# Optimization experiments

Measured on AMD Instinct MI355X. Metric: run time of the kernel, lower is better.

Reference implementation:

```python
import jax, jax.numpy as jnp
import numpy as np

B, T, C = 4, 2048, 1024
H, D = 16, 64  # num_heads, head_size; H*D == C


def setup_inputs() -> dict:
    key = jax.random.key(0)
    kx, kq, kk, kv = jax.random.split(key, 4)
    x = jax.random.normal(kx, (B, T, C), dtype=jnp.float32)
    # Per-head bias-free Q/K/V projection weights, stacked over heads.
    # Scale like torch Linear default init (~1/sqrt(fan_in)).
    s = 1.0 / np.sqrt(C)
    Wq = jax.random.normal(kq, (H, C, D), dtype=jnp.float32) * s
    Wk = jax.random.normal(kk, (H, C, D), dtype=jnp.float32) * s
    Wv = jax.random.normal(kv, (H, C, D), dtype=jnp.float32) * s
    return {"x": x, "Wq": Wq, "Wk": Wk, "Wv": Wv}


def reference(x, Wq, Wk, Wv):
    # Batched equivalent of the per-head Python loop:
    # each head: q = x @ Wq[h]; k = x @ Wk[h]; v = x @ Wv[h]
    q = jnp.einsum("btc,hcd->bhtd", x, Wq)
    k = jnp.einsum("bsc,hcd->bhsd", x, Wk)
    v = jnp.einsum("bsc,hcd->bhsd", x, Wv)
    scale = 1.0 / jnp.sqrt(jnp.asarray(D, dtype=x.dtype))
    scores = jnp.einsum("bhtd,bhsd->bhts", q, k) * scale  # [B,H,T,T]
    causal = jnp.tril(jnp.ones((T, T), dtype=bool))
    scores = jnp.where(causal[None, None], scores, jnp.asarray(-jnp.inf, scores.dtype))
    attn = jax.nn.softmax(scores, axis=-1)  # dropout=0 (inference)
    out = jnp.einsum("bhts,bhsd->bhtd", attn, v)
    # Concatenate heads on the last dim (head 0 first), matching torch.cat.
    return out.transpose(0, 2, 1, 3).reshape(B, T, H * D)
```

## Files before the change

### kernel.cpp

```cpp
#include <hip/hip_runtime.h>
#include <hip/hip_bf16.h>


typedef __attribute__((ext_vector_type(8))) short short8;
typedef __attribute__((ext_vector_type(4))) float f32x4;
typedef __attribute__((ext_vector_type(16))) float f32x16;

#define XB_OFF  64
#define WT_OFF  (64 + 8388608)
#define QKV_OFF (64 + 8388608 + 3145728)

__device__ __forceinline__ short f2bf(float f) {
    union { float f; unsigned u; } un; un.f = f;
    unsigned r = un.u + 0x7fffu + ((un.u >> 16) & 1u);
    return (short)(r >> 16);
}
__device__ __forceinline__ float bf2f(short v) {
    union { unsigned u; float f; } un; un.u = ((unsigned)(unsigned short)v) << 16;
    return un.f;
}
__device__ __forceinline__ unsigned cvtpk_bf16(float lo, float hi) {
    unsigned r;
    asm("v_cvt_pk_bf16_f32 %0, %1, %2" : "=v"(r) : "v"(lo), "v"(hi));
    return r;
}
__device__ __forceinline__ float fast_exp2(float x) {
    return __builtin_amdgcn_exp2f(x);
}

__device__ __forceinline__ int swz(int row, int colByte) {
    return row * 144 + (colByte ^ ((row & 56) << 1));
}

#define GLOAD16(gsrc, ldst)                                                       \
    __builtin_amdgcn_global_load_lds(                                             \
        (const __attribute__((address_space(1))) void*)(gsrc),                    \
        (__attribute__((address_space(3))) void*)(ldst), 16, 0, 0)

__global__ __launch_bounds__(256) void detect_dtype(const unsigned short* __restrict__ xs,
                                                    int* __restrict__ flag) {
    __shared__ int red[256];
    int t = threadIdx.x, cnt = 0;
    for (int i = t; i < 8192; i += 256) {
        unsigned e = (xs[i] >> 7) & 0xFFu;
        if (e >= 0xC0u) cnt++;
    }
    red[t] = cnt;
    __syncthreads();
    for (int s = 128; s > 0; s >>= 1) { if (t < s) red[t] += red[t + s]; __syncthreads(); }
    if (t == 0) flag[0] = (red[0] > 16) ? 1 : 0;
}

__global__ __launch_bounds__(256) void convert_x(const void* __restrict__ xin,
                                                 const int* __restrict__ flag,
                                                 short* __restrict__ xb) {
    const bool isf = (flag[0] != 0);
    const int n8 = 8388608 / 8;
    int i = blockIdx.x * 256 + threadIdx.x;
    const int stride = gridDim.x * 256;
    for (; i < n8; i += stride) {
        short8 v;
        if (isf) {
            const f32x4* xf = (const f32x4*)xin + i * 2;
            f32x4 a = xf[0], b = xf[1];
#pragma unroll
            for (int j = 0; j < 4; ++j) { v[j] = f2bf(a[j]); v[4 + j] = f2bf(b[j]); }
        } else {
            v = ((const short8*)xin)[i];
        }
        ((short8*)xb)[i] = v;
    }
}

__global__ __launch_bounds__(256) void transpose_w(const void* __restrict__ W0,
                                                   const void* __restrict__ W1,
                                                   const void* __restrict__ W2,
                                                   const int* __restrict__ flag,
                                                   short* __restrict__ Wt) {
    __shared__ short tile[64][72];
    const bool isf = (flag[0] != 0);
    const int s  = blockIdx.z;
    const void* W = (s == 0) ? W0 : (s == 1) ? W1 : W2;
    const int h  = blockIdx.y;
    const int c0 = blockIdx.x * 64;
    const int t  = threadIdx.x;
#pragma unroll
    for (int p = 0; p < 2; ++p) {
        int f8 = t + p * 256;
        int r  = f8 >> 3;
        int c8 = (f8 & 7) * 8;
        size_t base = (size_t)(h * 1024 + c0 + r) * 64 + c8;
        short8 v;
        if (isf) {
            const float* wf = (const float*)W + base;
#pragma unroll
            for (int j = 0; j < 8; ++j) v[j] = f2bf(wf[j]);
        } else {
            v = *(const short8*)((const short*)W + base);
        }
        *(short8*)&tile[r][c8] = v;
    }
    __syncthreads();
#pragma unroll
    for (int p = 0; p < 2; ++p) {
        int f8 = t + p * 256;
        int d  = f8 >> 3;
        int c8 = (f8 & 7) * 8;
        short8 v;
#pragma unroll
        for (int j = 0; j < 8; ++j) v[j] = tile[c8 + j][d];
        *(short8*)(Wt + (size_t)((s * 16 + h) * 64 + d) * 1024 + c0 + c8) = v;
    }
}

__global__ __launch_bounds__(256) void qkv_gemm(const short* __restrict__ xb,
                                                const short* __restrict__ Wt,
                                                short* __restrict__ qkv) {
    __shared__ short As[2 * 128 * 32];
    __shared__ short Bs[2 * 128 * 32];
    const int m0 = blockIdx.x * 128;
    const int n0 = blockIdx.y * 128;
    const int tid = threadIdx.x;
    const int wv = tid >> 6, ln = tid & 63;
    const int lr = ln & 15, lg = ln >> 4;
    const int wr = wv >> 1, wc = wv & 1;
    const int s = n0 >> 10;
    const int b = m0 >> 11;
    const float qs = (s == 0) ? 0.18033688f : 1.0f;

    const int srow = ln >> 2;
    const int sgrp = ((ln & 3) ^ ((ln >> 3) & 3)) * 8;
    const int roff = (lg ^ ((lr >> 1) & 3)) * 8;

    f32x4 acc[4][4] = {};
    const short* Abase = xb + (size_t)m0 * 1024;
    const short* Bbase = Wt + (size_t)n0 * 1024;

    for (int k0 = 0; k0 < 1024; k0 += 64) {
#pragma unroll
        for (int kh = 0; kh < 2; ++kh) {
            const int r0 = wv * 16, r1 = 64 + wv * 16;
            const int kc = k0 + kh * 32;
            GLOAD16(Abase + (size_t)(r0 + srow) * 1024 + kc + sgrp, As + kh * 4096 + r0 * 32);
            GLOAD16(Abase + (size_t)(r1 + srow) * 1024 + kc + sgrp, As + kh * 4096 + r1 * 32);
            GLOAD16(Bbase + (size_t)(r0 + srow) * 1024 + kc + sgrp, Bs + kh * 4096 + r0 * 32);
            GLOAD16(Bbase + (size_t)(r1 + srow) * 1024 + kc + sgrp, Bs + kh * 4096 + r1 * 32);
        }
        __syncthreads();
#pragma unroll
        for (int ks = 0; ks < 2; ++ks) {
            short8 af[4], bfr[4];
#pragma unroll
            for (int i = 0; i < 4; ++i)
                af[i] = *(const short8*)&As[ks * 4096 + (wr * 64 + i * 16 + lr) * 32 + roff];
#pragma unroll
            for (int i = 0; i < 4; ++i)
                bfr[i] = *(const short8*)&Bs[ks * 4096 + (wc * 64 + i * 16 + lr) * 32 + roff];
#pragma unroll
            for (int mi = 0; mi < 4; ++mi)
#pragma unroll
                for (int ni = 0; ni < 4; ++ni)
                    acc[mi][ni] = __builtin_amdgcn_mfma_f32_16x16x32_bf16(af[mi], bfr[ni], acc[mi][ni], 0, 0, 0);
        }
        __syncthreads();
    }

#pragma unroll
    for (int ni = 0; ni < 4; ++ni) {
        const int colbase = n0 + wc * 64 + ni * 16;
        const int h  = (colbase >> 6) & 15;
        const int d0 = colbase & 63;
        short* orow = qkv + (size_t)((s * 4 + b) * 16 + h) * 2048 * 64 + d0 + lr;
#pragma unroll
        for (int mi = 0; mi < 4; ++mi) {
            const size_t tb = (size_t)((m0 & 2047) + wr * 64 + mi * 16 + lg * 4) * 64;
#pragma unroll
            for (int r = 0; r < 4; ++r)
                orow[tb + (size_t)r * 64] = f2bf(acc[mi][ni][r] * qs);
        }
    }
}

#define BUILD_PW(s, stx, base) {                                             \
    unsigned P01 = cvtpk_bf16(stx[base + 0], stx[base + 1]);                 \
    unsigned P23 = cvtpk_bf16(stx[base + 2], stx[base + 3]);                 \
    unsigned P45 = cvtpk_bf16(stx[base + 4], stx[base + 5]);                 \
    unsigned P67 = cvtpk_bf16(stx[base + 6], stx[base + 7]);                 \
    asm volatile("v_permlane32_swap_b32 %0, %1" : "+v"(P01), "+v"(P45));     \
    asm volatile("v_permlane32_swap_b32 %0, %1" : "+v"(P23), "+v"(P67));     \
    pw[s][0] = P01; pw[s][1] = P23; pw[s][2] = P45; pw[s][3] = P67;          \
}

__device__ __forceinline__ void process_tile(const char* KsB, const char* VtB,
                                             short8 a0, short8 a1, short8 a2, short8 a3,
                                             float& ls,
                                             f32x16& o0, f32x16& o1,
                                             int qg, int kv0, bool diag,
                                             int q_, int hl) {
    short8 aq[4] = {a0, a1, a2, a3};
    f32x16 st0, st1;
#pragma unroll
    for (int r = 0; r < 16; ++r) { st0[r] = -14.0f; st1[r] = -14.0f; }
    __builtin_amdgcn_s_setprio(1);
#pragma unroll
    for (int s = 0; s < 4; ++s) {
        short8 kf0 = *(const short8*)(KsB + swz(q_,      s * 32 + hl * 16));
        short8 kf1 = *(const short8*)(KsB + swz(32 + q_, s * 32 + hl * 16));
        st0 = __builtin_amdgcn_mfma_f32_32x32x16_bf16(kf0, aq[s], st0, 0, 0, 0);
        st1 = __builtin_amdgcn_mfma_f32_32x32x16_bf16(kf1, aq[s], st1, 0, 0, 0);
    }
    __builtin_amdgcn_s_setprio(0);
    if (diag) {
#pragma unroll
        for (int r = 0; r < 16; ++r) {
            int key = kv0 + (r & 3) + 8 * (r >> 2) + 4 * hl;
            st0[r] = (key      <= qg) ? st0[r] : -1.0e30f;
            st1[r] = (key + 32 <= qg) ? st1[r] : -1.0e30f;
        }
    }
#pragma unroll
    for (int r = 0; r < 16; ++r) {
        st0[r] = fast_exp2(st0[r]);
        st1[r] = fast_exp2(st1[r]);
    }
    float tsum[8];
#pragma unroll
    for (int i = 0; i < 8; ++i)
        tsum[i] = (st0[i] + st0[i + 8]) + (st1[i] + st1[i + 8]);
    ls += ((tsum[0] + tsum[1]) + (tsum[2] + tsum[3]))
        + ((tsum[4] + tsum[5]) + (tsum[6] + tsum[7]));

    unsigned pw[4][4];
    BUILD_PW(0, st0, 0)
    BUILD_PW(1, st0, 8)
    BUILD_PW(2, st1, 0)
    BUILD_PW(3, st1, 8)
    __builtin_amdgcn_s_setprio(1);
#pragma unroll
    for (int s = 0; s < 4; ++s) {
        union { unsigned u[4]; short8 s8; } pb;
        pb.u[0] = pw[s][0]; pb.u[1] = pw[s][1]; pb.u[2] = pw[s][2]; pb.u[3] = pw[s][3];
        short8 v0 = *(const short8*)(VtB + swz(q_,      s * 32 + hl * 16));
        short8 v1 = *(const short8*)(VtB + swz(32 + q_, s * 32 + hl * 16));
        o0 = __builtin_amdgcn_mfma_f32_32x32x16_bf16(v0, pb.s8, o0, 0, 0, 0);
        o1 = __builtin_amdgcn_mfma_f32_32x32x16_bf16(v1, pb.s8, o1, 0, 0, 0);
    }
    __builtin_amdgcn_s_setprio(0);
}

#define EPILOGUE(oA, oB, lsv, q0base) {                                           \
    __syncthreads();                                                              \
    float inv = 1.0f / (lsv);                                                     \
    const int qlocal = w * 32 + q_;                                               \
    _Pragma("unroll")                                                             \
    for (int r = 0; r < 16; r += 2) {                                             \
        int d0 = (r & 3) + 8 * (r >> 2) + 4 * hl;                                 \
        *(unsigned*)(OtB + swz(qlocal, 2 * d0)) =                                 \
            cvtpk_bf16(oA[r] * inv, oA[r + 1] * inv);                             \
        *(unsigned*)(OtB + swz(qlocal, 2 * (32 + d0))) =                          \
            cvtpk_bf16(oB[r] * inv, oB[r + 1] * inv);                             \
    }                                                                             \
    __syncthreads();                                                              \
    _Pragma("unroll")                                                             \
    for (int i2 = 0; i2 < 4; ++i2) {                                              \
        int idx = i2 * 256 + tid;                                                 \
        int row = idx >> 3, cc8 = (idx & 7) * 8;                                  \
        short8 vch = *(const short8*)(OtB + swz(row, cc8 * 2));                   \
        size_t obase = (size_t)(b * 2048 + (q0base) + row) * 1024 + h * 64 + cc8; \
        if (isf) {                                                                \
            f32x4 lo2, hi2;                                                       \
            _Pragma("unroll")                                                     \
            for (int j = 0; j < 4; ++j) { lo2[j] = bf2f(vch[j]); hi2[j] = bf2f(vch[4 + j]); } \
            *(f32x4*)((float*)outp + obase)     = lo2;                            \
            *(f32x4*)((float*)outp + obase + 4) = hi2;                            \
        } else {                                                                  \
            *(short8*)((short*)outp + obase) = vch;                               \
        }                                                                         \
    }                                                                             \
}

__global__ __launch_bounds__(256, 2) void attn(const short* __restrict__ qkv,
                                               const int* __restrict__ flag,
                                               void* __restrict__ outp) {
    __shared__ short lds_all[2 * 9216];
    const bool isf = (flag[0] != 0);
    const int L    = (int)blockIdx.x;
    const int xcd  = L & 7;
    const int s_   = L >> 3;
    const int qbl  = s_ & 7;
    const int hb   = xcd * 8 + (s_ >> 3);
    const int b    = hb >> 4;
    const int h    = hb & 15;
    const int tid = threadIdx.x;
    const int w  = tid >> 6, l = tid & 63;
    const int q_ = l & 31;
    const int hl = l >> 5;
    const size_t BHTD = (size_t)4 * 16 * 2048 * 64;
    const short* Qb = qkv + (size_t)(b * 16 + h) * 2048 * 64;
    const short* Kb = Qb + BHTD;
    const short* Vb = Qb + 2 * BHTD;

    const int qbs0 = qbl, qbs1 = 15 - qbl;
    const int nt0 = 2 * qbs0 + 2, nt1 = 2 * qbs1 + 2;
    const int qg0 = qbs0 * 128 + w * 32 + q_;
    const int qg1 = qbs1 * 128 + w * 32 + q_;

    short8 aq0[4], aq1[4];
#pragma unroll
    for (int s = 0; s < 4; ++s) {
        aq0[s] = *(const short8*)(Qb + (size_t)qg0 * 64 + s * 16 + hl * 8);
        aq1[s] = *(const short8*)(Qb + (size_t)qg1 * 64 + s * 16 + hl * 8);
    }

    float ls0 = 0.f, ls1 = 0.f;
    f32x16 o00 = {}, o01 = {}, o10 = {}, o11 = {};

    const int kr = (tid >> 3) * 2;
    const int c8 = (tid & 7) * 8;
    short8 kreg[2], vreg[2];

    {
        kreg[0] = *(const short8*)(Kb + (size_t)kr * 64 + c8);
        kreg[1] = *(const short8*)(Kb + (size_t)(kr + 1) * 64 + c8);
        vreg[0] = *(const short8*)(Vb + (size_t)kr * 64 + c8);
        vreg[1] = *(const short8*)(Vb + (size_t)(kr + 1) * 64 + c8);
        char* KsN = (char*)lds_all;
        char* VtN = KsN + 9216;
        *(short8*)(KsN + swz(kr,     c8 * 2)) = kreg[0];
        *(short8*)(KsN + swz(kr + 1, c8 * 2)) = kreg[1];
#pragma unroll
        for (int j = 0; j < 8; ++j) {
            unsigned pv = (unsigned)(unsigned short)vreg[0][j]
                        | ((unsigned)(unsigned short)vreg[1][j] << 16);
            *(unsigned*)(VtN + swz(c8 + j, kr * 2)) = pv;
        }
    }

    for (int kt = 0; kt < nt1; ++kt) {
        const char* KsB = (const char*)lds_all + (kt & 1) * 18432;
        const char* VtB = KsB + 9216;
        __syncthreads();
        if (kt + 1 < nt1) {
            const short* Kn = Kb + (size_t)(kt + 1) * 4096;
            const short* Vn = Vb + (size_t)(kt + 1) * 4096;
            kreg[0] = *(const short8*)(Kn + (size_t)kr * 64 + c8);
            kreg[1] = *(const short8*)(Kn + (size_t)(kr + 1) * 64 + c8);
            vreg[0] = *(const short8*)(Vn + (size_t)kr * 64 + c8);
            vreg[1] = *(const short8*)(Vn + (size_t)(kr + 1) * 64 + c8);
        }
        const int kv0 = kt * 64;
        process_tile(KsB, VtB, aq1[0], aq1[1], aq1[2], aq1[3], ls1,
                     o10, o11, qg1, kv0, kt >= 2 * qbs1, q_, hl);
        if (kt < nt0)
            process_tile(KsB, VtB, aq0[0], aq0[1], aq0[2], aq0[3], ls0,
                         o00, o01, qg0, kv0, kt >= 2 * qbs0, q_, hl);
        if (kt + 1 < nt1) {
            char* KsN = (char*)lds_all + ((kt + 1) & 1) * 18432;
            char* VtN = KsN + 9216;
            *(short8*)(KsN + swz(kr,     c8 * 2)) = kreg[0];
            *(short8*)(KsN + swz(kr + 1, c8 * 2)) = kreg[1];
#pragma unroll
            for (int j = 0; j < 8; ++j) {
                unsigned pv = (unsigned)(unsigned short)vreg[0][j]
                            | ((unsigned)(unsigned short)vreg[1][j] << 16);
                *(unsigned*)(VtN + swz(c8 + j, kr * 2)) = pv;
            }
        }
    }

    ls0 += __shfl_xor(ls0, 32);
    ls1 += __shfl_xor(ls1, 32);
    char* const OtB = (char*)lds_all;
    EPILOGUE(o00, o01, ls0, qbs0 * 128)
    EPILOGUE(o10, o11, ls1, qbs1 * 128)
}

extern "C" void kernel_launch(void* const* d_in, const int* in_sizes, int n_in,
                              void* d_out, int out_size, void* d_ws, size_t ws_size,
                              hipStream_t stream) {
    short* ws   = (short*)d_ws;
    int*  flag  = (int*)d_ws;
    short* xb   = ws + XB_OFF;
    short* Wt   = ws + WT_OFF;
    short* qkvb = ws + QKV_OFF;

    dim3 blk(256);
    detect_dtype<<<1, blk, 0, stream>>>((const unsigned short*)d_in[0], flag);
    convert_x<<<dim3(1024), blk, 0, stream>>>(d_in[0], flag, xb);
    transpose_w<<<dim3(16, 16, 3), blk, 0, stream>>>(d_in[1], d_in[2], d_in[3], flag, Wt);
    qkv_gemm<<<dim3(64, 24), blk, 0, stream>>>(xb, Wt, qkvb);
    attn<<<dim3(512), blk, 0, stream>>>(qkvb, flag, d_out);
}
```

Measured before the change: 134.5 us.

## Fuse prep kernels into one launch and double-buffer QKV GEMM LDS tiles

Merges dtype detection, x conversion and weight transpose into a single prep kernel. Each block detects the dtype itself from a warp-level ballot over the first elements, which removes two kernel launches and their serial dependencies. The QKV GEMM now uses two LDS buffers so the global loads for the next K tile are issued while the current tile is being computed. This doubles LDS use per block, which may lower occupancy.

Result: slower. 146.6 us (+9.0%).

```diff
diff --git a/kernel.cpp b/kernel.cpp
--- a/kernel.cpp
+++ b/kernel.cpp
@@ -37,87 +37,87 @@
         (const __attribute__((address_space(1))) void*)(gsrc),                    \
         (__attribute__((address_space(3))) void*)(ldst), 16, 0, 0)
 
-__global__ __launch_bounds__(256) void detect_dtype(const unsigned short* __restrict__ xs,
-                                                    int* __restrict__ flag) {
-    __shared__ int red[256];
-    int t = threadIdx.x, cnt = 0;
-    for (int i = t; i < 8192; i += 256) {
-        unsigned e = (xs[i] >> 7) & 0xFFu;
-        if (e >= 0xC0u) cnt++;
-    }
-    red[t] = cnt;
-    __syncthreads();
-    for (int s = 128; s > 0; s >>= 1) { if (t < s) red[t] += red[t + s]; __syncthreads(); }
-    if (t == 0) flag[0] = (red[0] > 16) ? 1 : 0;
-}
-
-__global__ __launch_bounds__(256) void convert_x(const void* __restrict__ xin,
-                                                 const int* __restrict__ flag,
-                                                 short* __restrict__ xb) {
-    const bool isf = (flag[0] != 0);
-    const int n8 = 8388608 / 8;
-    int i = blockIdx.x * 256 + threadIdx.x;
-    const int stride = gridDim.x * 256;
-    for (; i < n8; i += stride) {
-        short8 v;
-        if (isf) {
-            const f32x4* xf = (const f32x4*)xin + i * 2;
-            f32x4 a = xf[0], b = xf[1];
-#pragma unroll
-            for (int j = 0; j < 4; ++j) { v[j] = f2bf(a[j]); v[4 + j] = f2bf(b[j]); }
-        } else {
-            v = ((const short8*)xin)[i];
-        }
-        ((short8*)xb)[i] = v;
-    }
-}
-
-__global__ __launch_bounds__(256) void transpose_w(const void* __restrict__ W0,
-                                                   const void* __restrict__ W1,
-                                                   const void* __restrict__ W2,
-                                                   const int* __restrict__ flag,
-                                                   short* __restrict__ Wt) {
+__global__ __launch_bounds__(256) void prep(const void* __restrict__ xin,
+                                            const void* __restrict__ W0,
+                                            const void* __restrict__ W1,
+                                            const void* __restrict__ W2,
+                                            int* __restrict__ flag,
+                                            short* __restrict__ xb,
+                                            short* __restrict__ Wt) {
     __shared__ short tile[64][72];
-    const bool isf = (flag[0] != 0);
-    const int s  = blockIdx.z;
-    const void* W = (s == 0) ? W0 : (s == 1) ? W1 : W2;
-    const int h  = blockIdx.y;
-    const int c0 = blockIdx.x * 64;
-    const int t  = threadIdx.x;
-#pragma unroll
-    for (int p = 0; p < 2; ++p) {
-        int f8 = t + p * 256;
-        int r  = f8 >> 3;
-        int c8 = (f8 & 7) * 8;
-        size_t base = (size_t)(h * 1024 + c0 + r) * 64 + c8;
-        short8 v;
-        if (isf) {
-            const float* wf = (const float*)W + base;
-#pragma unroll
-            for (int j = 0; j < 8; ++j) v[j] = f2bf(wf[j]);
-        } else {
-            v = *(const short8*)((const short*)W + base);
-        }
-        *(short8*)&tile[r][c8] = v;
-    }
-    __syncthreads();
-#pragma unroll
-    for (int p = 0; p < 2; ++p) {
-        int f8 = t + p * 256;
-        int d  = f8 >> 3;
-        int c8 = (f8 & 7) * 8;
-        short8 v;
-#pragma unroll
-        for (int j = 0; j < 8; ++j) v[j] = tile[c8 + j][d];
-        *(short8*)(Wt + (size_t)((s * 16 + h) * 64 + d) * 1024 + c0 + c8) = v;
+    const int tid  = threadIdx.x;
+    const int lane = tid & 63;
+    int cnt = 0;
+    const short8* xs8 = (const short8*)xin;
+#pragma unroll
+    for (int j = 0; j < 4; ++j) {
+        short8 v = xs8[lane * 4 + j];
+#pragma unroll
+        for (int e = 0; e < 8; ++e) {
+            unsigned ef = (((unsigned)(unsigned short)v[e]) >> 7) & 0xFFu;
+            cnt += (ef >= 0xC0u) ? 1 : 0;
+        }
+    }
+    const bool isf = __popcll(__ballot(cnt > 0)) > 32;
+    if (blockIdx.x == 0 && tid == 0) flag[0] = isf ? 1 : 0;
+
+    const int bid = (int)blockIdx.x;
+    if (bid < 1024) {
+        const int n8 = 8388608 / 8;
+        for (int i = bid * 256 + tid; i < n8; i += 1024 * 256) {
+            short8 v;
+            if (isf) {
+                const f32x4* xf = (const f32x4*)xin + i * 2;
+                f32x4 a = xf[0], b2 = xf[1];
+#pragma unroll
+                for (int j = 0; j < 4; ++j) { v[j] = f2bf(a[j]); v[4 + j] = f2bf(b2[j]); }
+            } else {
+                v = ((const short8*)xin)[i];
+            }
+            ((short8*)xb)[i] = v;
+        }
+    } else {
+        const int tb   = bid - 1024;
+        const int s    = tb >> 8;
+        const int rest = tb & 255;
+        const int h    = rest >> 4;
+        const int c0   = (rest & 15) * 64;
+        const void* W  = (s == 0) ? W0 : (s == 1) ? W1 : W2;
+#pragma unroll
+        for (int p = 0; p < 2; ++p) {
+            int f8 = tid + p * 256;
+            int r  = f8 >> 3;
+            int c8 = (f8 & 7) * 8;
+            size_t base = (size_t)(h * 1024 + c0 + r) * 64 + c8;
+            short8 v;
+            if (isf) {
+                const float* wf = (const float*)W + base;
+#pragma unroll
+                for (int j = 0; j < 8; ++j) v[j] = f2bf(wf[j]);
+            } else {
+                v = *(const short8*)((const short*)W + base);
+            }
+            *(short8*)&tile[r][c8] = v;
+        }
+        __syncthreads();
+#pragma unroll
+        for (int p = 0; p < 2; ++p) {
+            int f8 = tid + p * 256;
+            int d  = f8 >> 3;
+            int c8 = (f8 & 7) * 8;
+            short8 v;
+#pragma unroll
+            for (int j = 0; j < 8; ++j) v[j] = tile[c8 + j][d];
+            *(short8*)(Wt + (size_t)((s * 16 + h) * 64 + d) * 1024 + c0 + c8) = v;
+        }
     }
 }
 
 __global__ __launch_bounds__(256) void qkv_gemm(const short* __restrict__ xb,
                                                 const short* __restrict__ Wt,
                                                 short* __restrict__ qkv) {
-    __shared__ short As[2 * 128 * 32];
-    __shared__ short Bs[2 * 128 * 32];
+    __shared__ short As[2 * 8192];
+    __shared__ short Bs[2 * 8192];
     const int m0 = blockIdx.x * 128;
     const int n0 = blockIdx.y * 128;
     const int tid = threadIdx.x;
@@ -136,26 +136,37 @@
     const short* Abase = xb + (size_t)m0 * 1024;
     const short* Bbase = Wt + (size_t)n0 * 1024;
 
-    for (int k0 = 0; k0 < 1024; k0 += 64) {
-#pragma unroll
-        for (int kh = 0; kh < 2; ++kh) {
-            const int r0 = wv * 16, r1 = 64 + wv * 16;
-            const int kc = k0 + kh * 32;
-            GLOAD16(Abase + (size_t)(r0 + srow) * 1024 + kc + sgrp, As + kh * 4096 + r0 * 32);
-            GLOAD16(Abase + (size_t)(r1 + srow) * 1024 + kc + sgrp, As + kh * 4096 + r1 * 32);
-            GLOAD16(Bbase + (size_t)(r0 + srow) * 1024 + kc + sgrp, Bs + kh * 4096 + r0 * 32);
-            GLOAD16(Bbase + (size_t)(r1 + srow) * 1024 + kc + sgrp, Bs + kh * 4096 + r1 * 32);
-        }
-        __syncthreads();
+#define STAGE_QKV(bufp, k0v) {                                                    \
+    _Pragma("unroll")                                                             \
+    for (int kh = 0; kh < 2; ++kh) {                                              \
+        const int r0 = wv * 16, r1 = 64 + wv * 16;                                \
+        const int kc = (k0v) + kh * 32;                                           \
+        GLOAD16(Abase + (size_t)(r0 + srow) * 1024 + kc + sgrp,                   \
+                As + (bufp) * 8192 + kh * 4096 + r0 * 32);                        \
+        GLOAD16(Abase + (size_t)(r1 + srow) * 1024 + kc + sgrp,                   \
+                As + (bufp) * 8192 + kh * 4096 + r1 * 32);                        \
+        GLOAD16(Bbase + (size_t)(r0 + srow) * 1024 + kc + sgrp,                   \
+                Bs + (bufp) * 8192 + kh * 4096 + r0 * 32);                        \
+        GLOAD16(Bbase + (size_t)(r1 + srow) * 1024 + kc + sgrp,                   \
+                Bs + (bufp) * 8192 + kh * 4096 + r1 * 32);                        \
+    }                                                                             \
+}
+
+    STAGE_QKV(0, 0)
+    __syncthreads();
+
+    for (int t = 0; t < 16; ++t) {
+        const int cur = t & 1;
+        if (t + 1 < 16) STAGE_QKV(cur ^ 1, (t + 1) * 64)
 #pragma unroll
         for (int ks = 0; ks < 2; ++ks) {
             short8 af[4], bfr[4];
 #pragma unroll
             for (int i = 0; i < 4; ++i)
-                af[i] = *(const short8*)&As[ks * 4096 + (wr * 64 + i * 16 + lr) * 32 + roff];
+                af[i] = *(const short8*)&As[cur * 8192 + ks * 4096 + (wr * 64 + i * 16 + lr) * 32 + roff];
 #pragma unroll
             for (int i = 0; i < 4; ++i)
-                bfr[i] = *(const short8*)&Bs[ks * 4096 + (wc * 64 + i * 16 + lr) * 32 + roff];
+                bfr[i] = *(const short8*)&Bs[cur * 8192 + ks * 4096 + (wc * 64 + i * 16 + lr) * 32 + roff];
 #pragma unroll
             for (int mi = 0; mi < 4; ++mi)
 #pragma unroll
@@ -385,9 +396,7 @@
     short* qkvb = ws + QKV_OFF;
 
     dim3 blk(256);
-    detect_dtype<<<1, blk, 0, stream>>>((const unsigned short*)d_in[0], flag);
-    convert_x<<<dim3(1024), blk, 0, stream>>>(d_in[0], flag, xb);
-    transpose_w<<<dim3(16, 16, 3), blk, 0, stream>>>(d_in[1], d_in[2], d_in[3], flag, Wt);
+    prep<<<dim3(1792), blk, 0, stream>>>(d_in[0], d_in[1], d_in[2], d_in[3], flag, xb, Wt);
     qkv_gemm<<<dim3(64, 24), blk, 0, stream>>>(xb, Wt, qkvb);
     attn<<<dim3(512), blk, 0, stream>>>(qkvb, flag, d_out);
 }
```
